# Performance work log

Measured on AMD Instinct MI355X. Metric: run time of the kernel, lower is better.

## Reference

```python
import jax, jax.numpy as jnp
import numpy as np
import math

B, S, H = 2, 2048, 2048
NH, LD = 16, 512
HD = H // NH


def setup_inputs() -> dict:
    key = jax.random.key(0)
    ks = jax.random.split(key, 9)
    sc = 0.02
    return {
        "x": jax.random.normal(ks[0], (B, S, H), dtype=jnp.float32),
        "wq": jax.random.normal(ks[1], (H, H), dtype=jnp.float32) * sc,
        "bq": jnp.zeros((H,), dtype=jnp.float32),
        "wk_lat": jax.random.normal(ks[2], (H, LD), dtype=jnp.float32) * sc,
        "wv_lat": jax.random.normal(ks[3], (H, LD), dtype=jnp.float32) * sc,
        "wk": jax.random.normal(ks[4], (LD, H), dtype=jnp.float32) * sc,
        "wv": jax.random.normal(ks[5], (LD, H), dtype=jnp.float32) * sc,
        "wo": jax.random.normal(ks[6], (H, H), dtype=jnp.float32) * sc,
        "bo": jnp.zeros((H,), dtype=jnp.float32),
    }


def reference(x, wq, bq, wk_lat, wv_lat, wk, wv, wo, bo):
    b, s, _ = x.shape
    # projections
    q = (x @ wq + bq).reshape(b, s, NH, HD).transpose(0, 2, 1, 3)  # [B,NH,S,HD]
    k_lat = x @ wk_lat  # [B,S,LD]
    v_lat = x @ wv_lat
    k = (k_lat @ wk).reshape(b, s, NH, HD).transpose(0, 2, 1, 3)
    v = (v_lat @ wv).reshape(b, s, NH, HD).transpose(0, 2, 1, 3)
    # causal attention
    scores = jnp.einsum('bhqd,bhkd->bhqk', q, k) / math.sqrt(HD)
    mask = jnp.tril(jnp.ones((s, s), dtype=bool))  # True = keep
    scores = jnp.where(mask, scores, -jnp.inf)
    weights = jax.nn.softmax(scores, axis=-1)
    out = jnp.einsum('bhqk,bhkd->bhqd', weights, v)
    out = out.transpose(0, 2, 1, 3).reshape(b, s, H)
    return out @ wo + bo
```

## Files before the change

kernel.cpp:

```cpp
#include <hip/hip_runtime.h>
#include <hip/hip_bf16.h>

#define PB   2
#define PS   2048
#define PH   2048
#define PNH  16
#define PLD  512
#define PHD  128
#define PM   (PB * PS)
#define PNCAT 3072
#define ATT_SCALE 0.08838834764831845f

typedef __attribute__((ext_vector_type(8))) short bf16x8;
typedef __attribute__((ext_vector_type(4))) float f32x4;

__device__ __forceinline__ float bf2f(unsigned int h) {
    return __uint_as_float(h << 16);
}
__device__ __forceinline__ unsigned short f2bf(float f) {
    unsigned int u = __float_as_uint(f);
    u += 0x7FFFu + ((u >> 16) & 1u);
    return (unsigned short)(u >> 16);
}

__device__ __forceinline__ void gl_lds16(const unsigned short* g, unsigned short* l) {
    __builtin_amdgcn_global_load_lds(
        (const __attribute__((address_space(1))) unsigned int*)g,
        (__attribute__((address_space(3))) unsigned int*)l, 16, 0, 0);
}

__global__ __launch_bounds__(256) void cast_f32_bf16_kernel(
    const float* __restrict__ in, unsigned short* __restrict__ out, int n)
{
    int i = (blockIdx.x * 256 + threadIdx.x) * 4;
    if (i >= n) return;
    float4 f = *(const float4*)(in + i);
    unsigned int a = (unsigned int)f2bf(f.x) | ((unsigned int)f2bf(f.y) << 16);
    unsigned int b = (unsigned int)f2bf(f.z) | ((unsigned int)f2bf(f.w) << 16);
    *(uint2*)(out + i) = make_uint2(a, b);
}

__global__ __launch_bounds__(256) void transpose_cast_kernel(
    const float* __restrict__ in, unsigned short* __restrict__ out, int R, int C)
{
    __shared__ float tile[32][33];
    int tx = threadIdx.x, ty = threadIdx.y;
    int r0 = blockIdx.y * 32, c0 = blockIdx.x * 32;
#pragma unroll
    for (int i = 0; i < 32; i += 8)
        tile[ty + i][tx] = in[(size_t)(r0 + ty + i) * C + (c0 + tx)];
    __syncthreads();
#pragma unroll
    for (int i = 0; i < 32; i += 8)
        out[(size_t)(c0 + ty + i) * R + (r0 + tx)] = f2bf(tile[tx][ty + i]);
}

template<int EPI, bool HAS_BIAS>
__global__ __launch_bounds__(256) void gemm128_kernel(
    const unsigned short* __restrict__ A, int lda,
    const unsigned short* __restrict__ BT,
    const float* __restrict__ bias, int nbias,
    void* __restrict__ Cout, int ldc,
    int M, int N, int K)
{
    __shared__ __align__(16) unsigned short As[128 * 32];
    __shared__ __align__(16) unsigned short Bs[128 * 32];

    const int tid  = threadIdx.x;
    const int wave = tid >> 6;
    const int lane = tid & 63;
    const int wm = wave >> 1, wn = wave & 1;
    const int quad = lane >> 4, l15 = lane & 15;
    const int bm = blockIdx.y * 128, bn = blockIdx.x * 128;

    f32x4 acc[4][4] = {};

    const int srow = wave * 32 + (lane >> 2);
    const int scol = (lane & 3) * 8;
    const unsigned short* aG = A  + (size_t)(bm + srow) * lda + scol;
    const unsigned short* bG = BT + (size_t)(bn + srow) * K + scol;
    unsigned short* aL = &As[wave * 32 * 32];
    unsigned short* bL = &Bs[wave * 32 * 32];

    for (int k0 = 0; k0 < K; k0 += 32) {
        gl_lds16(aG + k0,                    aL);
        gl_lds16(aG + k0 + (size_t)16 * lda, aL + 16 * 32);
        gl_lds16(bG + k0,                    bL);
        gl_lds16(bG + k0 + (size_t)16 * K,   bL + 16 * 32);
        __syncthreads();
        bf16x8 af[4], bfr[4];
#pragma unroll
        for (int i = 0; i < 4; ++i) {
            af[i]  = *(const bf16x8*)&As[(wm * 64 + i * 16 + l15) * 32 + quad * 8];
            bfr[i] = *(const bf16x8*)&Bs[(wn * 64 + i * 16 + l15) * 32 + quad * 8];
        }
#pragma unroll
        for (int i = 0; i < 4; ++i)
#pragma unroll
            for (int j = 0; j < 4; ++j)
                acc[i][j] = __builtin_amdgcn_mfma_f32_16x16x32_bf16(af[i], bfr[j], acc[i][j], 0, 0, 0);
        __syncthreads();
    }

#pragma unroll
    for (int i = 0; i < 4; ++i)
#pragma unroll
        for (int j = 0; j < 4; ++j)
#pragma unroll
            for (int r = 0; r < 4; ++r) {
                int row = bm + wm * 64 + i * 16 + quad * 4 + r;
                int col = bn + wn * 64 + j * 16 + l15;
                float val = acc[i][j][r];
                if (HAS_BIAS && col < nbias) val += bias[col];
                if (EPI == 2) {
                    int bb = row >> 11, s = row & 2047, hh = col >> 7, d = col & 127;
                    size_t idx = ((size_t)((bb << 4) + hh) << 18) + ((size_t)(s >> 6) << 13)
                               + ((d >> 3) << 9) + ((s & 63) << 3) + (d & 7);
                    ((unsigned short*)Cout)[idx] = f2bf(val);
                } else if (EPI == 3) {
                    int bb = row >> 11, s = row & 2047, hh = col >> 7, d = col & 127;
                    size_t idx = ((size_t)((bb << 4) + hh) << 18) + ((size_t)(s >> 6) << 13)
                               + (((s >> 3) & 7) << 10) + (d << 3) + (s & 7);
                    ((unsigned short*)Cout)[idx] = f2bf(val);
                } else if (EPI == 1) {
                    ((float*)Cout)[(size_t)row * ldc + col] = val;
                } else {
                    ((unsigned short*)Cout)[(size_t)row * ldc + col] = f2bf(val);
                }
            }
}

__global__ __launch_bounds__(256) void flash_attn_mfma_kernel(
    const unsigned short* __restrict__ q,
    const unsigned short* __restrict__ kswz,
    const unsigned short* __restrict__ vswz,
    unsigned short* __restrict__ o)
{
    __shared__ __align__(16) unsigned short Kl[2][8192];
    __shared__ __align__(16) unsigned short Vl[8192];
    __shared__ __align__(16) unsigned short Ps[4][16][72];

    const int tid  = threadIdx.x;
    const int wave = tid >> 6;
    const int lane = tid & 63;
    const int quad = lane >> 4, l15 = lane & 15;

    const int bid = blockIdx.x;
    const int qt = 31 - (bid >> 5);
    const int bh = bid & 31;
    const int b  = bh >> 4, h = bh & 15;
    const int q0 = qt * 64;

    const unsigned short* qbase = q + (size_t)(b * PS + q0) * PNCAT + h * PHD;
    const unsigned short* kbase = kswz + ((size_t)bh << 18);
    const unsigned short* vbase = vswz + ((size_t)bh << 18);

    auto stageK = [&](int it, int buf) {
        const unsigned short* kt = kbase + ((size_t)it << 13);
#pragma unroll
        for (int j = 0; j < 4; ++j)
            gl_lds16(kt + (wave * 4 + j) * 512 + lane * 8, &Kl[buf][(wave * 4 + j) * 512]);
    };
    auto stageV = [&](int it) {
        const unsigned short* vt = vbase + ((size_t)it << 13);
#pragma unroll
        for (int j = 0; j < 4; ++j)
            gl_lds16(vt + (wave * 4 + j) * 512 + lane * 8, &Vl[(wave * 4 + j) * 512]);
    };

    bf16x8 aq[4];
#pragma unroll
    for (int kk = 0; kk < 4; ++kk)
        aq[kk] = *(const bf16x8*)(qbase + (size_t)(wave * 16 + l15) * PNCAT + kk * 32 + quad * 8);

    f32x4 oacc[8] = {};
    float m_prev[4], l_run[4];
#pragma unroll
    for (int r = 0; r < 4; ++r) { m_prev[r] = -1e30f; l_run[r] = 0.0f; }

    stageK(0, 0);

    for (int it = 0; it <= qt; ++it) {
        const int cur = it & 1;
        __syncthreads();
        stageV(it);
        if (it < qt) stageK(it + 1, cur ^ 1);

        f32x4 sacc[4] = {};
#pragma unroll
        for (int kk = 0; kk < 4; ++kk)
#pragma unroll
            for (int n = 0; n < 4; ++n) {
                bf16x8 bk = *(const bf16x8*)&Kl[cur][((kk * 4 + quad) * 64 + n * 16 + l15) * 8];
                sacc[n] = __builtin_amdgcn_mfma_f32_16x16x32_bf16(aq[kk], bk, sacc[n], 0, 0, 0);
            }

        float sraw[4][4];
        const bool diag = (it == qt);
#pragma unroll
        for (int n = 0; n < 4; ++n)
#pragma unroll
            for (int r = 0; r < 4; ++r) {
                float s = sacc[n][r] * ATT_SCALE;
                if (diag) {
                    int kg = n * 16 + l15;
                    int qg = wave * 16 + quad * 4 + r;
                    if (kg > qg) s = -1e30f;
                }
                sraw[n][r] = s;
            }

        float mx[4];
#pragma unroll
        for (int r = 0; r < 4; ++r)
            mx[r] = fmaxf(fmaxf(sraw[0][r], sraw[1][r]), fmaxf(sraw[2][r], sraw[3][r]));
#pragma unroll
        for (int sh = 1; sh < 16; sh <<= 1)
#pragma unroll
            for (int r = 0; r < 4; ++r)
                mx[r] = fmaxf(mx[r], __shfl_xor(mx[r], sh, 64));

        float alpha[4];
#pragma unroll
        for (int r = 0; r < 4; ++r) {
            float mn = fmaxf(m_prev[r], mx[r]);
            alpha[r] = __expf(m_prev[r] - mn);
            m_prev[r] = mn;
        }

        float rs[4] = {0, 0, 0, 0};
#pragma unroll
        for (int n = 0; n < 4; ++n)
#pragma unroll
            for (int r = 0; r < 4; ++r) {
                float p = __expf(sraw[n][r] - m_prev[r]);
                rs[r] += p;
                Ps[wave][quad * 4 + r][n * 16 + l15] = f2bf(p);
            }
#pragma unroll
        for (int sh = 1; sh < 16; sh <<= 1)
#pragma unroll
            for (int r = 0; r < 4; ++r)
                rs[r] += __shfl_xor(rs[r], sh, 64);
#pragma unroll
        for (int r = 0; r < 4; ++r)
            l_run[r] = l_run[r] * alpha[r] + rs[r];

#pragma unroll
        for (int n = 0; n < 8; ++n)
#pragma unroll
            for (int r = 0; r < 4; ++r)
                oacc[n][r] *= alpha[r];

        __syncthreads();

#pragma unroll
        for (int kk = 0; kk < 2; ++kk) {
            bf16x8 ap = *(const bf16x8*)&Ps[wave][l15][kk * 32 + quad * 8];
#pragma unroll
            for (int n = 0; n < 8; ++n) {
                bf16x8 bv = *(const bf16x8*)&Vl[((kk * 4 + quad) * 128 + n * 16 + l15) * 8];
                oacc[n] = __builtin_amdgcn_mfma_f32_16x16x32_bf16(ap, bv, oacc[n], 0, 0, 0);
            }
        }
    }

    float inv[4];
#pragma unroll
    for (int r = 0; r < 4; ++r) inv[r] = 1.0f / l_run[r];
#pragma unroll
    for (int n = 0; n < 8; ++n)
#pragma unroll
        for (int r = 0; r < 4; ++r) {
            int row = q0 + wave * 16 + quad * 4 + r;
            int col = h * PHD + n * 16 + l15;
            o[(size_t)(b * PS + row) * PH + col] = f2bf(oacc[n][r] * inv[r]);
        }
}

extern "C" void kernel_launch(void* const* d_in, const int* in_sizes, int n_in,
                              void* d_out, int out_size, void* d_ws, size_t ws_size,
                              hipStream_t stream)
{
    const float* x      = (const float*)d_in[0];
    const float* wq     = (const float*)d_in[1];
    const float* bq     = (const float*)d_in[2];
    const float* wk_lat = (const float*)d_in[3];
    const float* wv_lat = (const float*)d_in[4];
    const float* wk     = (const float*)d_in[5];
    const float* wv     = (const float*)d_in[6];
    const float* wo     = (const float*)d_in[7];
    const float* bo     = (const float*)d_in[8];
    float* out = (float*)d_out;

    char* ws = (char*)d_ws;
    size_t off = 0;
    auto alloc = [&](size_t bytes) -> void* {
        void* p = ws + off;
        off += (bytes + 255) & ~(size_t)255;
        return p;
    };
    unsigned short* xb    = (unsigned short*)alloc((size_t)PM * PH * 2);
    unsigned short* wcatT = (unsigned short*)alloc((size_t)PNCAT * PH * 2);
    unsigned short* wkT   = (unsigned short*)alloc((size_t)PH * PLD * 2);
    unsigned short* wvT   = (unsigned short*)alloc((size_t)PH * PLD * 2);
    unsigned short* woT   = (unsigned short*)alloc((size_t)PH * PH * 2);
    unsigned short* cat   = (unsigned short*)alloc((size_t)PM * PNCAT * 2);
    unsigned short* kswz  = (unsigned short*)alloc((size_t)PM * PH * 2);
    unsigned short* attn  = (unsigned short*)alloc((size_t)PM * PH * 2);
    unsigned short* vswz  = xb;

    unsigned short* wqT    = wcatT;
    unsigned short* wkLatT = wcatT + (size_t)PH * PH;
    unsigned short* wvLatT = wcatT + (size_t)(PH + PLD) * PH;

    dim3 tb(32, 8);

    cast_f32_bf16_kernel<<<(PM * PH) / 4 / 256, 256, 0, stream>>>(x, xb, PM * PH);
    transpose_cast_kernel<<<dim3(PH / 32,  PH / 32),  tb, 0, stream>>>(wq,     wqT,    PH,  PH);
    transpose_cast_kernel<<<dim3(PLD / 32, PH / 32),  tb, 0, stream>>>(wk_lat, wkLatT, PH,  PLD);
    transpose_cast_kernel<<<dim3(PLD / 32, PH / 32),  tb, 0, stream>>>(wv_lat, wvLatT, PH,  PLD);
    transpose_cast_kernel<<<dim3(PH / 32,  PLD / 32), tb, 0, stream>>>(wk,     wkT,    PLD, PH);
    transpose_cast_kernel<<<dim3(PH / 32,  PLD / 32), tb, 0, stream>>>(wv,     wvT,    PLD, PH);
    transpose_cast_kernel<<<dim3(PH / 32,  PH / 32),  tb, 0, stream>>>(wo,     woT,    PH,  PH);

    gemm128_kernel<0, true><<<dim3(PNCAT / 128, PM / 128), 256, 0, stream>>>(
        xb, PH, wcatT, bq, PH, cat, PNCAT, PM, PNCAT, PH);

    gemm128_kernel<2, false><<<dim3(PH / 128, PM / 128), 256, 0, stream>>>(
        cat + PH, PNCAT, wkT, nullptr, 0, kswz, 0, PM, PH, PLD);
    gemm128_kernel<3, false><<<dim3(PH / 128, PM / 128), 256, 0, stream>>>(
        cat + PH + PLD, PNCAT, wvT, nullptr, 0, vswz, 0, PM, PH, PLD);

    flash_attn_mfma_kernel<<<PB * PNH * (PS / 64), 256, 0, stream>>>(cat, kswz, vswz, attn);

    gemm128_kernel<1, true><<<dim3(PH / 128, PM / 128), 256, 0, stream>>>(
        attn, PH, woT, bo, PH, out, PH, PM, PH, PH);
}
```

Baseline: 409.5 us.

## Enlarge flash-attention query tile to 128 rows, drop K double buffering

Each workgroup now handles 128 query rows instead of 64, with each wave computing two 16-row MFMA slices. Every K/V tile loaded into LDS is therefore reused by twice as many queries, and the grid is halved. K double buffering is removed: K and V are loaded together, then a barrier waits for them before compute, so load latency is no longer overlapped with compute. The change also raises register pressure, gives fewer workgroups (512) to spread across CUs, and causes more causal imbalance per block.

```diff
diff --git a/kernel.cpp b/kernel.cpp
--- a/kernel.cpp
+++ b/kernel.cpp
@@ -136,9 +136,9 @@
     const unsigned short* __restrict__ vswz,
     unsigned short* __restrict__ o)
 {
-    __shared__ __align__(16) unsigned short Kl[2][8192];
+    __shared__ __align__(16) unsigned short Kl[8192];
     __shared__ __align__(16) unsigned short Vl[8192];
-    __shared__ __align__(16) unsigned short Ps[4][16][72];
+    __shared__ __align__(16) unsigned short Ps[4][32][72];
 
     const int tid  = threadIdx.x;
     const int wave = tid >> 6;
@@ -146,136 +146,156 @@
     const int quad = lane >> 4, l15 = lane & 15;
 
     const int bid = blockIdx.x;
-    const int qt = 31 - (bid >> 5);
+    const int qt = 15 - (bid >> 5);
     const int bh = bid & 31;
     const int b  = bh >> 4, h = bh & 15;
-    const int q0 = qt * 64;
+    const int q0 = qt * 128;
 
     const unsigned short* qbase = q + (size_t)(b * PS + q0) * PNCAT + h * PHD;
     const unsigned short* kbase = kswz + ((size_t)bh << 18);
     const unsigned short* vbase = vswz + ((size_t)bh << 18);
 
-    auto stageK = [&](int it, int buf) {
-        const unsigned short* kt = kbase + ((size_t)it << 13);
-#pragma unroll
-        for (int j = 0; j < 4; ++j)
-            gl_lds16(kt + (wave * 4 + j) * 512 + lane * 8, &Kl[buf][(wave * 4 + j) * 512]);
-    };
-    auto stageV = [&](int it) {
-        const unsigned short* vt = vbase + ((size_t)it << 13);
-#pragma unroll
-        for (int j = 0; j < 4; ++j)
-            gl_lds16(vt + (wave * 4 + j) * 512 + lane * 8, &Vl[(wave * 4 + j) * 512]);
-    };
-
-    bf16x8 aq[4];
-#pragma unroll
-    for (int kk = 0; kk < 4; ++kk)
-        aq[kk] = *(const bf16x8*)(qbase + (size_t)(wave * 16 + l15) * PNCAT + kk * 32 + quad * 8);
-
-    f32x4 oacc[8] = {};
-    float m_prev[4], l_run[4];
-#pragma unroll
-    for (int r = 0; r < 4; ++r) { m_prev[r] = -1e30f; l_run[r] = 0.0f; }
-
-    stageK(0, 0);
-
-    for (int it = 0; it <= qt; ++it) {
-        const int cur = it & 1;
+    bf16x8 aq[2][4];
+#pragma unroll
+    for (int mi = 0; mi < 2; ++mi)
+#pragma unroll
+        for (int kk = 0; kk < 4; ++kk)
+            aq[mi][kk] = *(const bf16x8*)(qbase
+                + (size_t)(wave * 32 + mi * 16 + l15) * PNCAT + kk * 32 + quad * 8);
+
+    f32x4 oacc[2][8] = {};
+    float m_prev[2][4], l_run[2][4];
+#pragma unroll
+    for (int mi = 0; mi < 2; ++mi)
+#pragma unroll
+        for (int r = 0; r < 4; ++r) { m_prev[mi][r] = -1e30f; l_run[mi][r] = 0.0f; }
+
+    const int niter = 2 * qt + 2;
+    for (int it = 0; it < niter; ++it) {
+        const int k0 = it * 64;
         __syncthreads();
-        stageV(it);
-        if (it < qt) stageK(it + 1, cur ^ 1);
-
-        f32x4 sacc[4] = {};
+        {
+            const unsigned short* kt = kbase + ((size_t)it << 13);
+            const unsigned short* vt = vbase + ((size_t)it << 13);
+#pragma unroll
+            for (int j = 0; j < 4; ++j) {
+                gl_lds16(kt + (wave * 4 + j) * 512 + lane * 8, &Kl[(wave * 4 + j) * 512]);
+                gl_lds16(vt + (wave * 4 + j) * 512 + lane * 8, &Vl[(wave * 4 + j) * 512]);
+            }
+        }
+        __syncthreads();
+
+        f32x4 sacc[2][4] = {};
 #pragma unroll
         for (int kk = 0; kk < 4; ++kk)
 #pragma unroll
             for (int n = 0; n < 4; ++n) {
-                bf16x8 bk = *(const bf16x8*)&Kl[cur][((kk * 4 + quad) * 64 + n * 16 + l15) * 8];
-                sacc[n] = __builtin_amdgcn_mfma_f32_16x16x32_bf16(aq[kk], bk, sacc[n], 0, 0, 0);
-            }
-
-        float sraw[4][4];
-        const bool diag = (it == qt);
-#pragma unroll
-        for (int n = 0; n < 4; ++n)
+                bf16x8 bk = *(const bf16x8*)&Kl[((kk * 4 + quad) * 64 + n * 16 + l15) * 8];
+                sacc[0][n] = __builtin_amdgcn_mfma_f32_16x16x32_bf16(aq[0][kk], bk, sacc[0][n], 0, 0, 0);
+                sacc[1][n] = __builtin_amdgcn_mfma_f32_16x16x32_bf16(aq[1][kk], bk, sacc[1][n], 0, 0, 0);
+            }
+
+        float sraw[2][4][4];
+        const bool diag = (it >= niter - 2);
+#pragma unroll
+        for (int mi = 0; mi < 2; ++mi)
+#pragma unroll
+            for (int n = 0; n < 4; ++n)
+#pragma unroll
+                for (int r = 0; r < 4; ++r) {
+                    float s = sacc[mi][n][r] * ATT_SCALE;
+                    if (diag) {
+                        int kg = k0 + n * 16 + l15;
+                        int qg = q0 + wave * 32 + mi * 16 + quad * 4 + r;
+                        if (kg > qg) s = -1e30f;
+                    }
+                    sraw[mi][n][r] = s;
+                }
+
+        float mx[2][4];
+#pragma unroll
+        for (int mi = 0; mi < 2; ++mi)
+#pragma unroll
+            for (int r = 0; r < 4; ++r)
+                mx[mi][r] = fmaxf(fmaxf(sraw[mi][0][r], sraw[mi][1][r]),
+                                  fmaxf(sraw[mi][2][r], sraw[mi][3][r]));
+#pragma unroll
+        for (int sh = 1; sh < 16; sh <<= 1)
+#pragma unroll
+            for (int mi = 0; mi < 2; ++mi)
+#pragma unroll
+                for (int r = 0; r < 4; ++r)
+                    mx[mi][r] = fmaxf(mx[mi][r], __shfl_xor(mx[mi][r], sh, 64));
+
+        float alpha[2][4];
+#pragma unroll
+        for (int mi = 0; mi < 2; ++mi)
 #pragma unroll
             for (int r = 0; r < 4; ++r) {
-                float s = sacc[n][r] * ATT_SCALE;
-                if (diag) {
-                    int kg = n * 16 + l15;
-                    int qg = wave * 16 + quad * 4 + r;
-                    if (kg > qg) s = -1e30f;
+                float mn = fmaxf(m_prev[mi][r], mx[mi][r]);
+                alpha[mi][r] = __expf(m_prev[mi][r] - mn);
+                m_prev[mi][r] = mn;
+            }
+
+        float rs[2][4] = {};
+#pragma unroll
+        for (int mi = 0; mi < 2; ++mi)
+#pragma unroll
+            for (int n = 0; n < 4; ++n)
+#pragma unroll
+                for (int r = 0; r < 4; ++r) {
+                    float p = __expf(sraw[mi][n][r] - m_prev[mi][r]);
+                    rs[mi][r] += p;
+                    Ps[wave][mi * 16 + quad * 4 + r][n * 16 + l15] = f2bf(p);
                 }
-                sraw[n][r] = s;
-            }
-
-        float mx[4];
-#pragma unroll
-        for (int r = 0; r < 4; ++r)
-            mx[r] = fmaxf(fmaxf(sraw[0][r], sraw[1][r]), fmaxf(sraw[2][r], sraw[3][r]));
 #pragma unroll
         for (int sh = 1; sh < 16; sh <<= 1)
 #pragma unroll
+            for (int mi = 0; mi < 2; ++mi)
+#pragma unroll
+                for (int r = 0; r < 4; ++r)
+                    rs[mi][r] += __shfl_xor(rs[mi][r], sh, 64);
+#pragma unroll
+        for (int mi = 0; mi < 2; ++mi)
+#pragma unroll
             for (int r = 0; r < 4; ++r)
-                mx[r] = fmaxf(mx[r], __shfl_xor(mx[r], sh, 64));
-
-        float alpha[4];
-#pragma unroll
-        for (int r = 0; r < 4; ++r) {
-            float mn = fmaxf(m_prev[r], mx[r]);
-            alpha[r] = __expf(m_prev[r] - mn);
-            m_prev[r] = mn;
-        }
-
-        float rs[4] = {0, 0, 0, 0};
-#pragma unroll
-        for (int n = 0; n < 4; ++n)
-#pragma unroll
-            for (int r = 0; r < 4; ++r) {
-                float p = __expf(sraw[n][r] - m_prev[r]);
-                rs[r] += p;
-                Ps[wave][quad * 4 + r][n * 16 + l15] = f2bf(p);
-            }
-#pragma unroll
-        for (int sh = 1; sh < 16; sh <<= 1)
-#pragma unroll
-            for (int r = 0; r < 4; ++r)
-                rs[r] += __shfl_xor(rs[r], sh, 64);
-#pragma unroll
-        for (int r = 0; r < 4; ++r)
-            l_run[r] = l_run[r] * alpha[r] + rs[r];
-
-#pragma unroll
-        for (int n = 0; n < 8; ++n)
-#pragma unroll
-            for (int r = 0; r < 4; ++r)
-                oacc[n][r] *= alpha[r];
-
-        __syncthreads();
+                l_run[mi][r] = l_run[mi][r] * alpha[mi][r] + rs[mi][r];
+
+#pragma unroll
+        for (int mi = 0; mi < 2; ++mi)
+#pragma unroll
+            for (int n = 0; n < 8; ++n)
+#pragma unroll
+                for (int r = 0; r < 4; ++r)
+                    oacc[mi][n][r] *= alpha[mi][r];
 
 #pragma unroll
         for (int kk = 0; kk < 2; ++kk) {
-            bf16x8 ap = *(const bf16x8*)&Ps[wave][l15][kk * 32 + quad * 8];
+            bf16x8 ap0 = *(const bf16x8*)&Ps[wave][     l15][kk * 32 + quad * 8];
+            bf16x8 ap1 = *(const bf16x8*)&Ps[wave][16 + l15][kk * 32 + quad * 8];
 #pragma unroll
             for (int n = 0; n < 8; ++n) {
                 bf16x8 bv = *(const bf16x8*)&Vl[((kk * 4 + quad) * 128 + n * 16 + l15) * 8];
-                oacc[n] = __builtin_amdgcn_mfma_f32_16x16x32_bf16(ap, bv, oacc[n], 0, 0, 0);
+                oacc[0][n] = __builtin_amdgcn_mfma_f32_16x16x32_bf16(ap0, bv, oacc[0][n], 0, 0, 0);
+                oacc[1][n] = __builtin_amdgcn_mfma_f32_16x16x32_bf16(ap1, bv, oacc[1][n], 0, 0, 0);
             }
         }
     }
 
-    float inv[4];
-#pragma unroll
-    for (int r = 0; r < 4; ++r) inv[r] = 1.0f / l_run[r];
-#pragma unroll
-    for (int n = 0; n < 8; ++n)
-#pragma unroll
-        for (int r = 0; r < 4; ++r) {
-            int row = q0 + wave * 16 + quad * 4 + r;
-            int col = h * PHD + n * 16 + l15;
-            o[(size_t)(b * PS + row) * PH + col] = f2bf(oacc[n][r] * inv[r]);
-        }
+#pragma unroll
+    for (int mi = 0; mi < 2; ++mi) {
+        float inv[4];
+#pragma unroll
+        for (int r = 0; r < 4; ++r) inv[r] = 1.0f / l_run[mi][r];
+#pragma unroll
+        for (int n = 0; n < 8; ++n)
+#pragma unroll
+            for (int r = 0; r < 4; ++r) {
+                int row = q0 + wave * 32 + mi * 16 + quad * 4 + r;
+                int col = h * PHD + n * 16 + l15;
+                o[(size_t)(b * PS + row) * PH + col] = f2bf(oacc[mi][n][r] * inv[r]);
+            }
+    }
 }
 
 extern "C" void kernel_launch(void* const* d_in, const int* in_sizes, int n_in,
@@ -332,7 +352,7 @@
     gemm128_kernel<3, false><<<dim3(PH / 128, PM / 128), 256, 0, stream>>>(
         cat + PH + PLD, PNCAT, wvT, nullptr, 0, vswz, 0, PM, PH, PLD);
 
-    flash_attn_mfma_kernel<<<PB * PNH * (PS / 64), 256, 0, stream>>>(cat, kswz, vswz, attn);
+    flash_attn_mfma_kernel<<<PB * PNH * (PS / 128), 256, 0, stream>>>(cat, kswz, vswz, attn);
 
     gemm128_kernel<1, true><<<dim3(PH / 128, PM / 128), 256, 0, stream>>>(
         attn, PH, woT, bo, PH, out, PH, PM, PH, PH);
```

New measurement: 450.9 us. 1.1x slower.
